# Performance work log

Hardware: AMD Instinct MI355X
Metric: run time of the kernel (lower is better)

The kernel has to match this reference:

```python
import jax, jax.numpy as jnp
import numpy as np
from jax import lax

T, H, F, E, K = 4096, 1024, 2048, 8, 2

def setup_inputs() -> dict:
    key = jax.random.key(0)
    k1, k2, k3, k4 = jax.random.split(key, 4)
    return {
        "hidden_states": jax.random.normal(k1, (T, H), jnp.float32),
        "gate_w": jax.random.normal(k2, (E, H), jnp.float32) * 0.02,
        "w1": jax.random.normal(k3, (E, 2 * F, H), jnp.float32) * 0.02,  # fused gate+up
        "w2": jax.random.normal(k4, (E, H, F), jnp.float32) * 0.02,      # down proj
        "top_k": K,
    }

def reference(hidden_states, gate_w, w1, w2, top_k):
    tokens = hidden_states.shape[0]
    # Router gate (Linear, no bias)
    router_logits = hidden_states @ gate_w.T                     # [T, E]
    probs = jax.nn.softmax(router_logits.astype(jnp.float32), axis=-1)
    topk_w, topk_idx = lax.top_k(probs, top_k)                   # [T, K]
    topk_w = topk_w / jnp.sum(topk_w, axis=-1, keepdims=True)    # renormalize
    # Dense combine weights [T, E] (zero for unselected experts)
    combine = jnp.zeros_like(probs).at[jnp.arange(tokens)[:, None], topk_idx].add(topk_w)
    combine = combine.astype(hidden_states.dtype)

    def expert_step(acc, ew):
        w1_e, w2_e, c_e = ew                                     # [2F,H], [H,F], [T]
        h = hidden_states @ w1_e.T                               # [T, 2F]
        g, u = jnp.split(h, 2, axis=-1)
        y = (jax.nn.silu(g) * u) @ w2_e.T                        # [T, H]
        return acc + c_e[:, None] * y, None

    acc0 = jnp.zeros_like(hidden_states)
    final_hidden_states, _ = lax.scan(expert_step, acc0, (w1, w2, combine.T))
    return final_hidden_states, router_logits
```

## Files before the change

### kernel.cpp

```cpp
#include <hip/hip_runtime.h>

#define T 4096
#define Hdim 1024
#define Fdim 2048
#define NE 8
#define TOPK 2
#define TK (T*TOPK)

typedef unsigned short ushort_t;
typedef __attribute__((ext_vector_type(8))) short bf16x8;
typedef __attribute__((ext_vector_type(4))) float floatx4;

__device__ __forceinline__ ushort_t f2bf(float f) {
    unsigned u = __float_as_uint(f);
    u += 0x7fff + ((u >> 16) & 1);
    return (ushort_t)(u >> 16);
}
__device__ __forceinline__ uint4 cvt8(const float4 a, const float4 b) {
    uint4 r;
    r.x = (unsigned)f2bf(a.x) | ((unsigned)f2bf(a.y) << 16);
    r.y = (unsigned)f2bf(a.z) | ((unsigned)f2bf(a.w) << 16);
    r.z = (unsigned)f2bf(b.x) | ((unsigned)f2bf(b.y) << 16);
    r.w = (unsigned)f2bf(b.z) | ((unsigned)f2bf(b.w) << 16);
    return r;
}
__device__ __forceinline__ void gld16(const ushort_t* g, short* l) {
    __builtin_amdgcn_global_load_lds((const __attribute__((address_space(1))) void*)g,
                                     (__attribute__((address_space(3))) void*)l, 16, 0, 0);
}

__global__ void init_kernel(int* __restrict__ counts) {
    if (threadIdx.x < NE) counts[threadIdx.x] = 0;
}

__global__ __launch_bounds__(256) void cvt_kernel(const float* __restrict__ src,
                                                  ushort_t* __restrict__ dst, long n8) {
    long stride = (long)gridDim.x * 256;
    for (long i = (long)blockIdx.x * 256 + threadIdx.x; i < n8; i += stride) {
        float4 a = *(const float4*)(src + i * 8);
        float4 b = *(const float4*)(src + i * 8 + 4);
        *(uint4*)(dst + i * 8) = cvt8(a, b);
    }
}

__global__ __launch_bounds__(64) void router_kernel(
    const float* __restrict__ hs, const float* __restrict__ gw,
    float* __restrict__ logits_out,
    int2* __restrict__ choice, float2* __restrict__ cwt)
{
    const int t = blockIdx.x;
    const int lane = threadIdx.x;

    float hreg[16];
#pragma unroll
    for (int i = 0; i < 16; ++i)
        hreg[i] = hs[(long)t * Hdim + lane + 64 * i];

    float acc[NE];
#pragma unroll
    for (int e = 0; e < NE; ++e) {
        float s = 0.f;
#pragma unroll
        for (int i = 0; i < 16; ++i)
            s += hreg[i] * gw[e * Hdim + lane + 64 * i];
#pragma unroll
        for (int off = 32; off > 0; off >>= 1)
            s += __shfl_xor(s, off, 64);
        acc[e] = s;
    }

    if (lane < NE) logits_out[t * NE + lane] = acc[lane];

    if (lane == 0) {
        int i1 = 0;
#pragma unroll
        for (int e = 1; e < NE; ++e) if (acc[e] > acc[i1]) i1 = e;
        int i2 = -1;
#pragma unroll
        for (int e = 0; e < NE; ++e) {
            if (e == i1) continue;
            if (i2 < 0 || acc[e] > acc[i2]) i2 = e;
        }
        float p2 = __expf(acc[i2] - acc[i1]);
        float z  = 1.f + p2;
        choice[t] = make_int2(i1, i2);
        cwt[t]    = make_float2(1.f / z, p2 / z);
    }
}

__global__ __launch_bounds__(256) void scatter_kernel(
    const int2* __restrict__ choice, const float2* __restrict__ cwt,
    int* __restrict__ counts, int* __restrict__ tok_slot, float* __restrict__ tok_wt)
{
    __shared__ int lhist[NE];
    __shared__ int lbase[NE];
    __shared__ int lpos[NE];
    const int tid = threadIdx.x;
    if (tid < NE) { lhist[tid] = 0; lpos[tid] = 0; }
    __syncthreads();

    const int t = blockIdx.x * 256 + tid;
    int2   ch = choice[t];
    float2 wv = cwt[t];
    atomicAdd(&lhist[ch.x], 1);
    atomicAdd(&lhist[ch.y], 1);
    __syncthreads();

    if (tid < NE) lbase[tid] = atomicAdd(&counts[tid], lhist[tid]);
    __syncthreads();

    int p1 = atomicAdd(&lpos[ch.x], 1);
    int p2 = atomicAdd(&lpos[ch.y], 1);
    int o1 = lbase[ch.x] + p1;
    int o2 = lbase[ch.y] + p2;
    tok_slot[ch.x * T + o1] = t * TOPK + 0;
    tok_wt [ch.x * T + o1] = wv.x;
    tok_slot[ch.y * T + o2] = t * TOPK + 1;
    tok_wt [ch.y * T + o2] = wv.y;
}

__global__ __launch_bounds__(256) void gemm1_kernel(
    const ushort_t* __restrict__ hsb, const ushort_t* __restrict__ w1b,
    const int* __restrict__ counts, const int* __restrict__ tok_slot,
    ushort_t* __restrict__ actb)
{
    const int e = blockIdx.z;
    const int cnt = counts[e];
    const int row0 = blockIdx.y * 128;
    if (row0 >= cnt) return;
    const int f0 = blockIdx.x * 64;

    __shared__ short As[128 * 32];
    __shared__ short Bs[128 * 32];
    __shared__ int slotLds[128];

    const int tid = threadIdx.x;
    if (tid < 128) {
        int idx = row0 + tid;
        slotLds[tid] = (idx < cnt) ? tok_slot[e * T + idx] : -1;
    }
    __syncthreads();

    const int rA0 = tid >> 2,      rA1 = 64 + (tid >> 2);
    const int seg = (tid & 3) * 8;
    int s0 = slotLds[rA0], s1 = slotLds[rA1];
    const ushort_t* srcA0 = hsb + (long)((s0 >= 0 ? (s0 >> 1) : 0)) * Hdim + seg;
    const ushort_t* srcA1 = hsb + (long)((s1 >= 0 ? (s1 >> 1) : 0)) * Hdim + seg;
    const ushort_t* srcB0 = w1b + ((long)e * 2 * Fdim + (f0 + rA0)) * Hdim + seg;
    const ushort_t* srcB1 = w1b + ((long)e * 2 * Fdim + Fdim + (f0 + rA0)) * Hdim + seg;

    const int lane = tid & 63;
    const int w = tid >> 6;
    const int wm = (w >> 1) * 64;
    const int wn = (w & 1) * 32;
    const int fr = lane & 15, fg = lane >> 4;

    floatx4 accg[4][2] = {};
    floatx4 accu[4][2] = {};

    for (int k0 = 0; k0 < Hdim; k0 += 32) {
        __syncthreads();
        gld16(srcA0 + k0, &As[tid * 8]);
        gld16(srcA1 + k0, &As[(256 + tid) * 8]);
        gld16(srcB0 + k0, &Bs[tid * 8]);
        gld16(srcB1 + k0, &Bs[(256 + tid) * 8]);
        __syncthreads();

        bf16x8 a[4], g[2], u[2];
#pragma unroll
        for (int ms = 0; ms < 4; ++ms)
            a[ms] = *(bf16x8*)&As[(wm + ms * 16 + fr) * 32 + fg * 8];
#pragma unroll
        for (int ns = 0; ns < 2; ++ns) {
            g[ns] = *(bf16x8*)&Bs[(wn + ns * 16 + fr) * 32 + fg * 8];
            u[ns] = *(bf16x8*)&Bs[(64 + wn + ns * 16 + fr) * 32 + fg * 8];
        }
#pragma unroll
        for (int ms = 0; ms < 4; ++ms)
#pragma unroll
            for (int ns = 0; ns < 2; ++ns) {
                accg[ms][ns] = __builtin_amdgcn_mfma_f32_16x16x32_bf16(a[ms], g[ns], accg[ms][ns], 0, 0, 0);
                accu[ms][ns] = __builtin_amdgcn_mfma_f32_16x16x32_bf16(a[ms], u[ns], accu[ms][ns], 0, 0, 0);
            }
    }

#pragma unroll
    for (int ms = 0; ms < 4; ++ms)
#pragma unroll
        for (int ns = 0; ns < 2; ++ns)
#pragma unroll
            for (int j = 0; j < 4; ++j) {
                int m = wm + ms * 16 + fg * 4 + j;
                int slot = slotLds[m];
                if (slot >= 0) {
                    int fcol = f0 + wn + ns * 16 + fr;
                    float gv = accg[ms][ns][j];
                    float uv = accu[ms][ns][j];
                    float av = (gv / (1.f + __expf(-gv))) * uv;
                    actb[(long)slot * Fdim + fcol] = f2bf(av);
                }
            }
}

__global__ __launch_bounds__(256) void gemm2_kernel(
    const ushort_t* __restrict__ actb, const ushort_t* __restrict__ w2b,
    const int* __restrict__ counts, const int* __restrict__ tok_slot,
    const float* __restrict__ tok_wt, float* __restrict__ partial)
{
    const int e = blockIdx.z;
    const int cnt = counts[e];
    const int row0 = blockIdx.y * 128;
    if (row0 >= cnt) return;
    const int h0 = blockIdx.x * 128;

    __shared__ short As[128 * 32];
    __shared__ short Bs[128 * 32];
    __shared__ int   slotLds[128];
    __shared__ float wtLds[128];

    const int tid = threadIdx.x;
    if (tid < 128) {
        int idx = row0 + tid;
        bool ok = idx < cnt;
        slotLds[tid] = ok ? tok_slot[e * T + idx] : -1;
        wtLds[tid]   = ok ? tok_wt [e * T + idx] : 0.f;
    }
    __syncthreads();

    const int rA0 = tid >> 2, rA1 = 64 + (tid >> 2);
    const int seg = (tid & 3) * 8;
    int s0 = slotLds[rA0], s1 = slotLds[rA1];
    const ushort_t* srcA0 = actb + (long)(s0 >= 0 ? s0 : 0) * Fdim + seg;
    const ushort_t* srcA1 = actb + (long)(s1 >= 0 ? s1 : 0) * Fdim + seg;
    const ushort_t* srcB0 = w2b + ((long)e * Hdim + (h0 + rA0)) * Fdim + seg;
    const ushort_t* srcB1 = w2b + ((long)e * Hdim + (h0 + rA1)) * Fdim + seg;

    const int lane = tid & 63;
    const int w = tid >> 6;
    const int wm = (w >> 1) * 64;
    const int wn = (w & 1) * 64;
    const int fr = lane & 15, fg = lane >> 4;

    floatx4 acc[4][4] = {};

    for (int k0 = 0; k0 < Fdim; k0 += 32) {
        __syncthreads();
        gld16(srcA0 + k0, &As[tid * 8]);
        gld16(srcA1 + k0, &As[(256 + tid) * 8]);
        gld16(srcB0 + k0, &Bs[tid * 8]);
        gld16(srcB1 + k0, &Bs[(256 + tid) * 8]);
        __syncthreads();

        bf16x8 a[4], b[4];
#pragma unroll
        for (int ms = 0; ms < 4; ++ms)
            a[ms] = *(bf16x8*)&As[(wm + ms * 16 + fr) * 32 + fg * 8];
#pragma unroll
        for (int ns = 0; ns < 4; ++ns)
            b[ns] = *(bf16x8*)&Bs[(wn + ns * 16 + fr) * 32 + fg * 8];
#pragma unroll
        for (int ms = 0; ms < 4; ++ms)
#pragma unroll
            for (int ns = 0; ns < 4; ++ns)
                acc[ms][ns] = __builtin_amdgcn_mfma_f32_16x16x32_bf16(a[ms], b[ns], acc[ms][ns], 0, 0, 0);
    }

#pragma unroll
    for (int ms = 0; ms < 4; ++ms)
#pragma unroll
        for (int ns = 0; ns < 4; ++ns)
#pragma unroll
            for (int j = 0; j < 4; ++j) {
                int m = wm + ms * 16 + fg * 4 + j;
                int slot = slotLds[m];
                if (slot >= 0) {
                    int hcol = h0 + wn + ns * 16 + fr;
                    partial[(long)slot * Hdim + hcol] = acc[ms][ns][j] * wtLds[m];
                }
            }
}

__global__ __launch_bounds__(256) void combine_kernel(
    const float* __restrict__ partial, float* __restrict__ out)
{
    long i = (long)blockIdx.x * 256 + threadIdx.x;
    int t  = (int)(i / (Hdim / 4));
    int h4 = (int)(i % (Hdim / 4));
    const float4 p0 = *(const float4*)&partial[(long)(2 * t    ) * Hdim + h4 * 4];
    const float4 p1 = *(const float4*)&partial[(long)(2 * t + 1) * Hdim + h4 * 4];
    float4 s;
    s.x = p0.x + p1.x; s.y = p0.y + p1.y; s.z = p0.z + p1.z; s.w = p0.w + p1.w;
    *(float4*)&out[(long)t * Hdim + h4 * 4] = s;
}

extern "C" void kernel_launch(void* const* d_in, const int* in_sizes, int n_in,
                              void* d_out, int out_size, void* d_ws, size_t ws_size,
                              hipStream_t stream)
{
    const float* hs = (const float*)d_in[0];
    const float* gw = (const float*)d_in[1];
    const float* w1 = (const float*)d_in[2];
    const float* w2 = (const float*)d_in[3];

    float* out        = (float*)d_out;
    float* logits_out = out + (long)T * Hdim;

    char* ws = (char*)d_ws;
    size_t off = 0;
    int* counts = (int*)(ws + off);          off += 256;
    int* tok_slot = (int*)(ws + off);        off += (size_t)NE * T * sizeof(int);
    float* tok_wt = (float*)(ws + off);      off += (size_t)NE * T * sizeof(float);
    off = (off + 255) & ~(size_t)255;
    ushort_t* hsb = (ushort_t*)(ws + off);   off += (size_t)T * Hdim * sizeof(ushort_t);
    off = (off + 255) & ~(size_t)255;
    char* w1region = ws + off;               off += (size_t)NE * 2 * Fdim * Hdim * sizeof(ushort_t);
    ushort_t* w1b = (ushort_t*)w1region;
    ushort_t* w2b = (ushort_t*)w1region;
    float* partial = (float*)(w1region + (size_t)NE * Hdim * Fdim * sizeof(ushort_t));
    off = (off + 255) & ~(size_t)255;
    ushort_t* actb = (ushort_t*)(ws + off);  off += (size_t)TK * Fdim * sizeof(ushort_t);
    int2*   choice = (int2*)actb;
    float2* cwt    = (float2*)((char*)actb + (size_t)T * sizeof(int2));

    init_kernel<<<1, 64, 0, stream>>>(counts);
    cvt_kernel<<<1024, 256, 0, stream>>>(hs, hsb, (long)T * Hdim / 8);
    cvt_kernel<<<2048, 256, 0, stream>>>(w1, w1b, (long)NE * 2 * Fdim * Hdim / 8);
    router_kernel<<<T, 64, 0, stream>>>(hs, gw, logits_out, choice, cwt);
    scatter_kernel<<<T / 256, 256, 0, stream>>>(choice, cwt, counts, tok_slot, tok_wt);
    gemm1_kernel<<<dim3(Fdim / 64, T / 128, NE), 256, 0, stream>>>(hsb, w1b, counts, tok_slot, actb);
    cvt_kernel<<<2048, 256, 0, stream>>>(w2, w2b, (long)NE * Hdim * Fdim / 8);
    gemm2_kernel<<<dim3(Hdim / 128, T / 128, NE), 256, 0, stream>>>(actb, w2b, counts, tok_slot, tok_wt, partial);
    combine_kernel<<<(int)((long)T * Hdim / 4 / 256), 256, 0, stream>>>(partial, out);
}
```

Baseline: 440.9 us.

## Fuse conversion launches, fold counter init into router, widen gemm2 to 8 waves

Merges the hidden-state and w1 fp32-to-bf16 conversions into a single launch and drops grid-stride loops in favour of one element per thread. Removes the separate counts-init kernel by zeroing counts in the first router block. Reworks gemm2 to use 512 threads with 8 waves each computing a 64x32 sub-tile, so each thread issues one A and one B global-to-LDS load per k step and holds fewer accumulators. This aims to cut launch overhead and improve latency hiding in gemm2, at the cost of more threads contending for barriers.

```diff
diff --git a/kernel.cpp b/kernel.cpp
--- a/kernel.cpp
+++ b/kernel.cpp
@@ -29,27 +29,40 @@
                                      (__attribute__((address_space(3))) void*)l, 16, 0, 0);
 }
 
-__global__ void init_kernel(int* __restrict__ counts) {
-    if (threadIdx.x < NE) counts[threadIdx.x] = 0;
+__global__ __launch_bounds__(256) void cvt2_kernel(
+    const float* __restrict__ srcA, ushort_t* __restrict__ dstA, long n8A,
+    const float* __restrict__ srcB, ushort_t* __restrict__ dstB)
+{
+    long i = (long)blockIdx.x * 256 + threadIdx.x;
+    if (i < n8A) {
+        float4 a = *(const float4*)(srcA + i * 8);
+        float4 b = *(const float4*)(srcA + i * 8 + 4);
+        *(uint4*)(dstA + i * 8) = cvt8(a, b);
+    } else {
+        long j = i - n8A;
+        float4 a = *(const float4*)(srcB + j * 8);
+        float4 b = *(const float4*)(srcB + j * 8 + 4);
+        *(uint4*)(dstB + j * 8) = cvt8(a, b);
+    }
 }
 
 __global__ __launch_bounds__(256) void cvt_kernel(const float* __restrict__ src,
-                                                  ushort_t* __restrict__ dst, long n8) {
-    long stride = (long)gridDim.x * 256;
-    for (long i = (long)blockIdx.x * 256 + threadIdx.x; i < n8; i += stride) {
-        float4 a = *(const float4*)(src + i * 8);
-        float4 b = *(const float4*)(src + i * 8 + 4);
-        *(uint4*)(dst + i * 8) = cvt8(a, b);
-    }
+                                                  ushort_t* __restrict__ dst)
+{
+    long i = (long)blockIdx.x * 256 + threadIdx.x;
+    float4 a = *(const float4*)(src + i * 8);
+    float4 b = *(const float4*)(src + i * 8 + 4);
+    *(uint4*)(dst + i * 8) = cvt8(a, b);
 }
 
 __global__ __launch_bounds__(64) void router_kernel(
     const float* __restrict__ hs, const float* __restrict__ gw,
     float* __restrict__ logits_out,
-    int2* __restrict__ choice, float2* __restrict__ cwt)
+    int2* __restrict__ choice, float2* __restrict__ cwt, int* __restrict__ counts)
 {
     const int t = blockIdx.x;
     const int lane = threadIdx.x;
+    if (t == 0 && lane < NE) counts[lane] = 0;
 
     float hreg[16];
 #pragma unroll
@@ -202,7 +215,7 @@
             }
 }
 
-__global__ __launch_bounds__(256) void gemm2_kernel(
+__global__ __launch_bounds__(512) void gemm2_kernel(
     const ushort_t* __restrict__ actb, const ushort_t* __restrict__ w2b,
     const int* __restrict__ counts, const int* __restrict__ tok_slot,
     const float* __restrict__ tok_wt, float* __restrict__ partial)
@@ -227,48 +240,44 @@
     }
     __syncthreads();
 
-    const int rA0 = tid >> 2, rA1 = 64 + (tid >> 2);
+    const int r   = tid >> 2;
     const int seg = (tid & 3) * 8;
-    int s0 = slotLds[rA0], s1 = slotLds[rA1];
-    const ushort_t* srcA0 = actb + (long)(s0 >= 0 ? s0 : 0) * Fdim + seg;
-    const ushort_t* srcA1 = actb + (long)(s1 >= 0 ? s1 : 0) * Fdim + seg;
-    const ushort_t* srcB0 = w2b + ((long)e * Hdim + (h0 + rA0)) * Fdim + seg;
-    const ushort_t* srcB1 = w2b + ((long)e * Hdim + (h0 + rA1)) * Fdim + seg;
+    int s = slotLds[r];
+    const ushort_t* srcA = actb + (long)(s >= 0 ? s : 0) * Fdim + seg;
+    const ushort_t* srcB = w2b + ((long)e * Hdim + (h0 + r)) * Fdim + seg;
 
     const int lane = tid & 63;
     const int w = tid >> 6;
-    const int wm = (w >> 1) * 64;
-    const int wn = (w & 1) * 64;
+    const int wm = (w >> 2) * 64;
+    const int wn = (w & 3) * 32;
     const int fr = lane & 15, fg = lane >> 4;
 
-    floatx4 acc[4][4] = {};
+    floatx4 acc[4][2] = {};
 
     for (int k0 = 0; k0 < Fdim; k0 += 32) {
         __syncthreads();
-        gld16(srcA0 + k0, &As[tid * 8]);
-        gld16(srcA1 + k0, &As[(256 + tid) * 8]);
-        gld16(srcB0 + k0, &Bs[tid * 8]);
-        gld16(srcB1 + k0, &Bs[(256 + tid) * 8]);
+        gld16(srcA + k0, &As[tid * 8]);
+        gld16(srcB + k0, &Bs[tid * 8]);
         __syncthreads();
 
-        bf16x8 a[4], b[4];
+        bf16x8 a[4], b[2];
 #pragma unroll
         for (int ms = 0; ms < 4; ++ms)
             a[ms] = *(bf16x8*)&As[(wm + ms * 16 + fr) * 32 + fg * 8];
 #pragma unroll
-        for (int ns = 0; ns < 4; ++ns)
+        for (int ns = 0; ns < 2; ++ns)
             b[ns] = *(bf16x8*)&Bs[(wn + ns * 16 + fr) * 32 + fg * 8];
 #pragma unroll
         for (int ms = 0; ms < 4; ++ms)
 #pragma unroll
-            for (int ns = 0; ns < 4; ++ns)
+            for (int ns = 0; ns < 2; ++ns)
                 acc[ms][ns] = __builtin_amdgcn_mfma_f32_16x16x32_bf16(a[ms], b[ns], acc[ms][ns], 0, 0, 0);
     }
 
 #pragma unroll
     for (int ms = 0; ms < 4; ++ms)
 #pragma unroll
-        for (int ns = 0; ns < 4; ++ns)
+        for (int ns = 0; ns < 2; ++ns)
 #pragma unroll
             for (int j = 0; j < 4; ++j) {
                 int m = wm + ms * 16 + fg * 4 + j;
@@ -322,13 +331,15 @@
     int2*   choice = (int2*)actb;
     float2* cwt    = (float2*)((char*)actb + (size_t)T * sizeof(int2));
 
-    init_kernel<<<1, 64, 0, stream>>>(counts);
-    cvt_kernel<<<1024, 256, 0, stream>>>(hs, hsb, (long)T * Hdim / 8);
-    cvt_kernel<<<2048, 256, 0, stream>>>(w1, w1b, (long)NE * 2 * Fdim * Hdim / 8);
-    router_kernel<<<T, 64, 0, stream>>>(hs, gw, logits_out, choice, cwt);
+    const long n8_hs = (long)T * Hdim / 8;
+    const long n8_w1 = (long)NE * 2 * Fdim * Hdim / 8;
+    const long n8_w2 = (long)NE * Hdim * Fdim / 8;
+
+    cvt2_kernel<<<(int)((n8_hs + n8_w1) / 256), 256, 0, stream>>>(hs, hsb, n8_hs, w1, w1b);
+    router_kernel<<<T, 64, 0, stream>>>(hs, gw, logits_out, choice, cwt, counts);
     scatter_kernel<<<T / 256, 256, 0, stream>>>(choice, cwt, counts, tok_slot, tok_wt);
     gemm1_kernel<<<dim3(Fdim / 64, T / 128, NE), 256, 0, stream>>>(hsb, w1b, counts, tok_slot, actb);
-    cvt_kernel<<<2048, 256, 0, stream>>>(w2, w2b, (long)NE * Hdim * Fdim / 8);
-    gemm2_kernel<<<dim3(Hdim / 128, T / 128, NE), 256, 0, stream>>>(actb, w2b, counts, tok_slot, tok_wt, partial);
+    cvt_kernel<<<(int)(n8_w2 / 256), 256, 0, stream>>>(w2, w2b);
+    gemm2_kernel<<<dim3(Hdim / 128, T / 128, NE), 512, 0, stream>>>(actb, w2b, counts, tok_slot, tok_wt, partial);
     combine_kernel<<<(int)((long)T * Hdim / 4 / 256), 256, 0, stream>>>(partial, out);
 }
```

Result: no change. 437.3 us (-0.8%).
